# Optimization experiments

Hardware: AMD Instinct MI355X
Metric: run time of the kernel (lower is better)

Reference implementation:

```python
import jax, jax.numpy as jnp
from jax import lax
import numpy as np

B = 8192
NUM_CTX = 300; NUM_STN = 300; NUM_GPE = 20; NUM_GPI = 2; NUM_OUT = 20
FF_DIM = 20; FF_STEPS = 20; STN_ITERS = 50
ETA_GPE = 1.0; ETA_STN = 1.0 / 3.0; ETA_GPI = 0.1
A1 = 1.0; A2 = 1.0; THETAD1 = 0.0; THETAD2 = 0.0
UNITS = (64, 128, 64)

_SPECS = [("vf0", UNITS[0], NUM_CTX), ("vf1", UNITS[1], UNITS[0]), ("vf2", UNITS[2], UNITS[1]), ("vf3", 1, UNITS[2]),
          ("jd1", FF_DIM, NUM_CTX), ("jd2", FF_DIM, NUM_CTX), ("kd1", FF_DIM, NUM_CTX), ("kd2", FF_DIM, NUM_CTX),
          ("sg", NUM_GPE, NUM_STN), ("gs", NUM_STN, NUM_GPE), ("glat", NUM_GPE, NUM_GPE), ("slat", NUM_STN, NUM_STN),
          ("d1gpi", NUM_GPI, FF_DIM), ("stngpi", NUM_GPI, NUM_STN),
          ("ih", 4 * NUM_OUT, NUM_GPI), ("hh", 4 * NUM_OUT, NUM_OUT)]


def _lin_init(k, out_d, in_d):
    kw, kb = jax.random.split(k)
    bound = 1.0 / np.sqrt(in_d)
    w = jax.random.uniform(kw, (out_d, in_d), minval=-bound, maxval=bound, dtype=jnp.float32)
    b = jax.random.uniform(kb, (out_d,), minval=-bound, maxval=bound, dtype=jnp.float32)
    return w, b


def setup_inputs() -> dict:
    key = jax.random.key(0)
    ks = iter(jax.random.split(key, 40))
    inp = {}
    inp["stimulus"] = jax.random.normal(next(ks), (B, NUM_CTX), dtype=jnp.float32)
    inp["deltavf"] = jax.random.normal(next(ks), (B, 1), dtype=jnp.float32)
    inp["hx0"] = jax.random.uniform(next(ks), (B, NUM_OUT), dtype=jnp.float32)
    inp["cx0"] = jax.random.uniform(next(ks), (B, NUM_OUT), dtype=jnp.float32)
    for name, o, i in _SPECS:
        w, b = _lin_init(next(ks), o, i)
        inp["w_" + name] = w
        inp["b_" + name] = b
    return inp


def _lin(x, w, b):
    return x @ w.T + b


def _lstm_cell(x, h, c, w_ih, b_ih, w_hh, b_hh):
    gates = _lin(x, w_ih, b_ih) + _lin(h, w_hh, b_hh)
    i, f, g, o = jnp.split(gates, 4, axis=-1)  # torch LSTMCell gate order
    c_new = jax.nn.sigmoid(f) * c + jax.nn.sigmoid(i) * jnp.tanh(g)
    h_new = jax.nn.sigmoid(o) * jnp.tanh(c_new)
    return h_new, c_new


def reference(stimulus, deltavf, hx0, cx0,
              w_vf0, b_vf0, w_vf1, b_vf1, w_vf2, b_vf2, w_vf3, b_vf3,
              w_jd1, b_jd1, w_jd2, b_jd2, w_kd1, b_kd1, w_kd2, b_kd2,
              w_sg, b_sg, w_gs, b_gs, w_glat, b_glat, w_slat, b_slat,
              w_d1gpi, b_d1gpi, w_stngpi, b_stngpi,
              w_ih, b_ih, w_hh, b_hh):
    bsz = stimulus.shape[0]
    # value function head
    h = jax.nn.relu(_lin(stimulus, w_vf0, b_vf0))
    h = jax.nn.relu(_lin(h, w_vf1, b_vf1))
    h = jax.nn.relu(_lin(h, w_vf2, b_vf2))
    vt = jnp.tanh(_lin(h, w_vf3, b_vf3))  # [B, 1]

    lamd1 = jax.nn.sigmoid(A1 * (deltavf - THETAD1))  # [B, 1]
    lamd2 = jax.nn.sigmoid(A2 * (deltavf - THETAD2))  # [B, 1]

    # loop-invariant striatal drives (computed every iter in torch, same value)
    J_D1 = _lin(stimulus, w_jd1, b_jd1)
    J_D2 = _lin(stimulus, w_jd2, b_jd2)
    K_D1 = _lin(stimulus, w_kd1, b_kd1)
    K_D2 = _lin(stimulus, w_kd2, b_kd2)

    def ff_step(carry, _):
        v1, v2 = carry
        v1 = jax.nn.sigmoid(lamd1 * (J_D1 * (1.0 - v1) + (1.0 - K_D1) * v1))
        v2 = jax.nn.sigmoid(lamd2 * (J_D2 * (1.0 - v2) + (1.0 - K_D2) * v2))
        return (v1, v2), None

    z_ff = jnp.zeros((bsz, FF_DIM), dtype=stimulus.dtype)
    (V_D1, V_D2), _ = lax.scan(ff_step, (z_ff, z_ff), None, length=FF_STEPS)

    V_GPi_DP = _lin(V_D1, w_d1gpi, b_d1gpi)  # [B, num_gpi]

    def stn_step(carry, _):
        xgpe, xstn, vstn, vgpi, hx, cx = carry
        xgpe = xgpe + ETA_GPE * (-xgpe + _lin(vstn, w_sg, b_sg) + _lin(xgpe, w_glat, b_glat) - V_D2)
        xstn = xstn + ETA_STN * (-xstn + _lin(xgpe, w_gs, b_gs) + _lin(vstn, w_slat, b_slat))
        vstn = jnp.tanh(lamd2 * xstn)
        V_GPi_IP = lamd2 * _lin(vstn, w_stngpi, b_stngpi)
        vgpi = vgpi + ETA_GPI * (-vgpi - V_GPi_DP + 2.0 * V_GPi_IP)
        hx, cx = _lstm_cell(-vgpi, hx, cx, w_ih, b_ih, w_hh, b_hh)
        return (xgpe, xstn, vstn, vgpi, hx, cx), None

    carry0 = (jnp.zeros((bsz, NUM_GPE), dtype=stimulus.dtype),
              jnp.zeros((bsz, NUM_STN), dtype=stimulus.dtype),
              jnp.zeros((bsz, NUM_STN), dtype=stimulus.dtype),  # tanh(lamd2*0) = 0
              jnp.zeros((bsz, NUM_GPI), dtype=stimulus.dtype),
              hx0, cx0)
    carry, _ = lax.scan(stn_step, carry0, None, length=STN_ITERS)
    hx = carry[4]
    return hx, vt
```

## Files before the change

kernel.cpp:

```cpp
#include <hip/hip_runtime.h>


typedef _Float16 f16_t;
typedef _Float16 f16x8 __attribute__((ext_vector_type(8)));
typedef _Float16 f16x4 __attribute__((ext_vector_type(4)));
typedef float floatx4 __attribute__((ext_vector_type(4)));

#define BTOT 8192
#define BM   32
#define NTHR 512
#define NBLK 256
#define VSTR 328
#define XST  32

struct Params {
  const float *stimulus, *deltavf, *hx0, *cx0;
  const float *w_vf0, *b_vf0, *w_vf1, *b_vf1, *w_vf2, *b_vf2, *w_vf3, *b_vf3;
  const float *w_jd1, *b_jd1, *w_jd2, *b_jd2, *w_kd1, *b_kd1, *w_kd2, *b_kd2;
  const float *w_sg, *b_sg, *w_gs, *b_gs, *w_glat, *b_glat, *w_slat, *b_slat;
  const float *w_d1gpi, *b_d1gpi, *w_stngpi, *b_stngpi;
  const float *w_ih, *b_ih, *w_hh, *b_hh;
  float* out;
};

struct __align__(16) Smem {
  f16_t vstn[BM * VSTR];
  f16_t xgpe[2][BM * XST];
  f16_t hxf[BM * XST];
  f16_t wB2[21 * 512];
  union {
    f16_t h1f[BM * 128];
    float scr[2560];
    float gates[BM * 80];
  } u;
  float h0f[BM * 64];
  float V_D2f[BM * 20];
  float cxL[BM * 20], hxL[BM * 20];
  float bsumS[304];
  float bsg[20];
  float bihh[80], wih0[80], wih1[80];
  float DPs[BM * 2], vgpis[BM * 2], lamS[BM];
};

__device__ __forceinline__ float rcp_f(float x) { return __builtin_amdgcn_rcpf(x); }
__device__ __forceinline__ float sigm_fast(float x) { return rcp_f(1.f + __expf(-x)); }
__device__ __forceinline__ float tanh_fast(float x) { return 1.f - 2.f * rcp_f(1.f + __expf(2.f * x)); }

__device__ __forceinline__ f16x8 ldfrag(const float* row, int k0, int kmax, bool valid) {
  float4 z = make_float4(0.f, 0.f, 0.f, 0.f);
  int nv = valid ? (kmax - k0) : 0;
  float4 f0 = (nv >= 4) ? *(const float4*)(row + k0) : z;
  float4 f1 = (nv >= 8) ? *(const float4*)(row + k0 + 4) : z;
  f16x8 r;
  r[0] = (f16_t)f0.x; r[1] = (f16_t)f0.y; r[2] = (f16_t)f0.z; r[3] = (f16_t)f0.w;
  r[4] = (f16_t)f1.x; r[5] = (f16_t)f1.y; r[6] = (f16_t)f1.z; r[7] = (f16_t)f1.w;
  return r;
}

__global__ __launch_bounds__(NTHR, 2) void bg_main(Params P) {
  __shared__ Smem S;
  const int tid  = threadIdx.x;
  const int lane = tid & 63;
  const int wv   = tid >> 6;
  const int q    = lane >> 4;
  const int cl   = lane & 15;
  const int row0 = blockIdx.x * BM;
  const floatx4 zf = {0.f, 0.f, 0.f, 0.f};

  if (tid < BM) S.lamS[tid] = sigm_fast(P.deltavf[row0 + tid]);
  for (int i = tid; i < BM * 2; i += NTHR) S.vgpis[i] = 0.f;
  for (int i = tid; i < BM * VSTR; i += NTHR) S.vstn[i] = (f16_t)0.f;
  for (int i = tid; i < 2 * BM * XST; i += NTHR) ((f16_t*)S.xgpe)[i] = (f16_t)0.f;
  for (int i = tid; i < BM * XST; i += NTHR) {
    int m = i >> 5, j = i & 31;
    S.hxf[i] = (j < 20) ? (f16_t)P.hx0[row0 * 20 + m * 20 + j] : (f16_t)0.f;
  }
  for (int i = tid; i < BM * 20; i += NTHR) {
    S.cxL[i] = P.cx0[row0 * 20 + i];
    S.hxL[i] = P.hx0[row0 * 20 + i];
  }
  for (int i = tid; i < 21 * 512; i += NTHR) {
    int t = i >> 9, l = (i >> 3) & 63, jj = i & 7;
    int c2 = l & 15, k = ((l >> 4) << 3) + jj;
    float v = 0.f;
    if (t < 19) { int n = t * 16 + c2; if (n < 300 && k < 20) v = P.w_gs[n * 20 + k]; }
    else        { int g = (t - 19) * 16 + c2; if (g < 20 && k < 20) v = P.w_glat[g * 20 + k]; }
    S.wB2[i] = (f16_t)v;
  }
  for (int i = tid; i < 304; i += NTHR) S.bsumS[i] = (i < 300) ? (P.b_slat[i] + P.b_gs[i]) : 0.f;
  for (int i = tid; i < 20; i += NTHR)  S.bsg[i] = P.b_sg[i] + P.b_glat[i];
  for (int i = tid; i < 80; i += NTHR) {
    S.bihh[i] = P.b_ih[i] + P.b_hh[i];
    S.wih0[i] = P.w_ih[i * 2 + 0];
    S.wih1[i] = P.w_ih[i * 2 + 1];
  }

  {
    int o = tid & 63, mb = (tid >> 6) * 4;
    const float4* wr = (const float4*)(P.w_vf0 + o * 300);
    float bias = P.b_vf0[o], a[4];
#pragma unroll
    for (int u2 = 0; u2 < 4; ++u2) a[u2] = bias;
    for (int kq = 0; kq < 75; ++kq) {
      float4 w = wr[kq];
#pragma unroll
      for (int u2 = 0; u2 < 4; ++u2) {
        float4 v = *(const float4*)(P.stimulus + (size_t)(row0 + mb + u2) * 300 + kq * 4);
        a[u2] = fmaf(v.x, w.x, a[u2]); a[u2] = fmaf(v.y, w.y, a[u2]);
        a[u2] = fmaf(v.z, w.z, a[u2]); a[u2] = fmaf(v.w, w.w, a[u2]);
      }
    }
#pragma unroll
    for (int u2 = 0; u2 < 4; ++u2) S.h0f[(mb + u2) * 64 + o] = fmaxf(a[u2], 0.f);
  }
  __syncthreads();
  {
    int o = tid & 127, mb = (tid >> 7) * 8;
    const float* wr = P.w_vf1 + o * 64;
    float bias = P.b_vf1[o], a[8];
#pragma unroll
    for (int u2 = 0; u2 < 8; ++u2) a[u2] = bias;
    for (int k = 0; k < 64; ++k) {
      float w = wr[k];
#pragma unroll
      for (int u2 = 0; u2 < 8; ++u2) a[u2] = fmaf(S.h0f[(mb + u2) * 64 + k], w, a[u2]);
    }
#pragma unroll
    for (int u2 = 0; u2 < 8; ++u2) S.u.h1f[(mb + u2) * 128 + o] = (f16_t)fmaxf(a[u2], 0.f);
  }
  __syncthreads();
  {
    int o = tid & 63, mb = (tid >> 6) * 4;
    const float* wr = P.w_vf2 + o * 128;
    float bias = P.b_vf2[o], a[4];
#pragma unroll
    for (int u2 = 0; u2 < 4; ++u2) a[u2] = bias;
    for (int k = 0; k < 128; ++k) {
      float w = wr[k];
#pragma unroll
      for (int u2 = 0; u2 < 4; ++u2) a[u2] = fmaf((float)S.u.h1f[(mb + u2) * 128 + k], w, a[u2]);
    }
#pragma unroll
    for (int u2 = 0; u2 < 4; ++u2) S.h0f[(mb + u2) * 64 + o] = fmaxf(a[u2], 0.f);
  }
  __syncthreads();
  {
    int oid = tid & 127, mb = (tid >> 7) * 8;
    if (oid < 80) {
      int which = oid / 20, o = oid - which * 20;
      const float *wp, *bp;
      if (which == 0)      { wp = P.w_jd1; bp = P.b_jd1; }
      else if (which == 1) { wp = P.w_jd2; bp = P.b_jd2; }
      else if (which == 2) { wp = P.w_kd1; bp = P.b_kd1; }
      else                 { wp = P.w_kd2; bp = P.b_kd2; }
      float bias = bp[o], a[8];
#pragma unroll
      for (int u2 = 0; u2 < 8; ++u2) a[u2] = bias;
      for (int kq = 0; kq < 75; ++kq) {
        float4 w = *(const float4*)(wp + o * 300 + kq * 4);
#pragma unroll
        for (int u2 = 0; u2 < 8; ++u2) {
          float4 v = *(const float4*)(P.stimulus + (size_t)(row0 + mb + u2) * 300 + kq * 4);
          a[u2] = fmaf(v.x, w.x, a[u2]); a[u2] = fmaf(v.y, w.y, a[u2]);
          a[u2] = fmaf(v.z, w.z, a[u2]); a[u2] = fmaf(v.w, w.w, a[u2]);
        }
      }
#pragma unroll
      for (int u2 = 0; u2 < 8; ++u2) S.u.scr[which * 640 + (mb + u2) * 20 + o] = a[u2];
    }
    if (tid < BM) {
      float a = P.b_vf3[0];
      for (int k = 0; k < 64; ++k) a = fmaf(S.h0f[tid * 64 + k], P.w_vf3[k], a);
      P.out[(size_t)BTOT * 20 + row0 + tid] = tanh_fast(a);
    }
  }
  __syncthreads();
  for (int i = tid; i < BM * 20; i += NTHR) {
    int m = i / 20;
    float j1 = S.u.scr[i],        j2 = S.u.scr[640 + i];
    float k1 = S.u.scr[1280 + i], k2 = S.u.scr[1920 + i];
    float L = S.lamS[m], v1 = 0.f, v2 = 0.f;
    for (int s = 0; s < 20; ++s) {
      v1 = sigm_fast(L * (j1 * (1.f - v1) + (1.f - k1) * v1));
      v2 = sigm_fast(L * (j2 * (1.f - v2) + (1.f - k2) * v2));
    }
    S.V_D2f[i] = v2;
    S.h0f[i] = v1;
  }
  __syncthreads();
  if (tid < BM * 2) {
    int m = tid >> 1, p2 = tid & 1;
    float a = P.b_d1gpi[p2];
    for (int o = 0; o < 20; ++o) a = fmaf(S.h0f[m * 20 + o], P.w_d1gpi[p2 * 20 + o], a);
    S.DPs[tid] = a;
  }
  __syncthreads();

  f16x8 Wfr[30];
  if (wv < 7) {
#pragma unroll
    for (int j = 0; j < 3; ++j) {
      int t = wv + 7 * j;
      if (t < 19) {
        int n = t * 16 + cl;
#pragma unroll
        for (int c = 0; c < 10; ++c)
          Wfr[j * 10 + c] = ldfrag(P.w_slat + (size_t)(n < 300 ? n : 0) * 300, c * 32 + q * 8, 300, n < 300);
      } else {
        int g = (t - 19) * 16 + cl;
#pragma unroll
        for (int c = 0; c < 10; ++c)
          Wfr[j * 10 + c] = ldfrag(P.w_sg + (size_t)(g < 20 ? g : 0) * 300, c * 32 + q * 8, 300, g < 20);
      }
    }
  } else {
#pragma unroll
    for (int c = 0; c < 10; ++c)
      Wfr[c] = ldfrag(P.w_stngpi + (size_t)(cl < 2 ? cl : 0) * 300, c * 32 + q * 8, 300, cl < 2);
#pragma unroll
    for (int gt = 0; gt < 5; ++gt)
      Wfr[10 + gt] = ldfrag(P.w_hh + (size_t)(gt * 16 + cl) * 20, q * 8, 20, true);
    f16x8 z;
#pragma unroll
    for (int e = 0; e < 8; ++e) z[e] = (f16_t)0.f;
#pragma unroll
    for (int c = 15; c < 30; ++c) Wfr[c] = z;
  }
  const float bstn0 = P.b_stngpi[0], bstn1 = P.b_stngpi[1];

  float xs[3][2][4];
#pragma unroll
  for (int j = 0; j < 3; ++j)
#pragma unroll
    for (int mf = 0; mf < 2; ++mf)
#pragma unroll
      for (int r = 0; r < 4; ++r) xs[j][mf][r] = 0.f;

  const int cm = lane >> 1, cj0 = (lane & 1) * 10;

  auto consume = [&]() {
    floatx4 ip0 = zf, ip1 = zf;
#pragma unroll
    for (int c = 0; c < 10; ++c) {
      f16x8 b0 = *(const f16x8*)&S.vstn[cl * VSTR + c * 32 + q * 8];
      f16x8 b1 = *(const f16x8*)&S.vstn[(16 + cl) * VSTR + c * 32 + q * 8];
      ip0 = __builtin_amdgcn_mfma_f32_16x16x32_f16(Wfr[c], b0, ip0, 0, 0, 0);
      ip1 = __builtin_amdgcn_mfma_f32_16x16x32_f16(Wfr[c], b1, ip1, 0, 0, 0);
    }
    if (q == 0) {
#pragma unroll
      for (int mf = 0; mf < 2; ++mf) {
        int batch = cl + 16 * mf;
        float lm = S.lamS[batch];
#pragma unroll
        for (int p = 0; p < 2; ++p) {
          float raw = (mf ? ip1[p] : ip0[p]) + (p ? bstn1 : bstn0);
          int idx = batch * 2 + p;
          float v = S.vgpis[idx];
          v = v + 0.1f * (-v - S.DPs[idx] + 2.f * (lm * raw));
          S.vgpis[idx] = v;
        }
      }
    }
    f16x8 h0 = *(const f16x8*)&S.hxf[cl * XST + q * 8];
    f16x8 h1 = *(const f16x8*)&S.hxf[(16 + cl) * XST + q * 8];
    float vA0 = S.vgpis[cl * 2], vA1 = S.vgpis[cl * 2 + 1];
    float vB0 = S.vgpis[(cl + 16) * 2], vB1 = S.vgpis[(cl + 16) * 2 + 1];
#pragma unroll
    for (int gt = 0; gt < 5; ++gt) {
      floatx4 gA = __builtin_amdgcn_mfma_f32_16x16x32_f16(Wfr[10 + gt], h0, zf, 0, 0, 0);
      floatx4 gB = __builtin_amdgcn_mfma_f32_16x16x32_f16(Wfr[10 + gt], h1, zf, 0, 0, 0);
      int gb = gt * 16 + q * 4;
      floatx4 bi = *(const floatx4*)&S.bihh[gb];
      floatx4 w0 = *(const floatx4*)&S.wih0[gb];
      floatx4 w1 = *(const floatx4*)&S.wih1[gb];
#pragma unroll
      for (int r = 0; r < 4; ++r) {
        gA[r] += bi[r] - w0[r] * vA0 - w1[r] * vA1;
        gB[r] += bi[r] - w0[r] * vB0 - w1[r] * vB1;
      }
      *(floatx4*)&S.u.gates[cl * 80 + gb] = gA;
      *(floatx4*)&S.u.gates[(cl + 16) * 80 + gb] = gB;
    }
#pragma unroll
    for (int u2 = 0; u2 < 10; ++u2) {
      int j = cj0 + u2;
      float gi = S.u.gates[cm * 80 + j];
      float gf = S.u.gates[cm * 80 + 20 + j];
      float gg = S.u.gates[cm * 80 + 40 + j];
      float go = S.u.gates[cm * 80 + 60 + j];
      float cx = S.cxL[cm * 20 + j];
      float cn = sigm_fast(gf) * cx + sigm_fast(gi) * tanh_fast(gg);
      S.cxL[cm * 20 + j] = cn;
      float hn = sigm_fast(go) * tanh_fast(cn);
      S.hxL[cm * 20 + j] = hn;
      S.hxf[cm * XST + j] = (f16_t)hn;
    }
  };

  for (int it = 0; it < 50; ++it) {
    const int po = it & 1, pn = po ^ 1;
    floatx4 acc[3][2];
#pragma unroll
    for (int j = 0; j < 3; ++j) { acc[j][0] = zf; acc[j][1] = zf; }

    if (wv < 7) {
#pragma unroll
      for (int c = 0; c < 10; ++c) {
        f16x8 b0 = *(const f16x8*)&S.vstn[cl * VSTR + c * 32 + q * 8];
        f16x8 b1 = *(const f16x8*)&S.vstn[(16 + cl) * VSTR + c * 32 + q * 8];
#pragma unroll
        for (int j = 0; j < 3; ++j) {
          acc[j][0] = __builtin_amdgcn_mfma_f32_16x16x32_f16(Wfr[j * 10 + c], b0, acc[j][0], 0, 0, 0);
          acc[j][1] = __builtin_amdgcn_mfma_f32_16x16x32_f16(Wfr[j * 10 + c], b1, acc[j][1], 0, 0, 0);
        }
      }
      if (wv >= 5) {
        f16x8 Wg = *(const f16x8*)&S.wB2[(wv + 14) * 512 + lane * 8];
        f16x8 g0 = *(const f16x8*)&S.xgpe[po][cl * XST + q * 8];
        f16x8 g1 = *(const f16x8*)&S.xgpe[po][(16 + cl) * XST + q * 8];
        acc[2][0] = __builtin_amdgcn_mfma_f32_16x16x32_f16(Wg, g0, acc[2][0], 0, 0, 0);
        acc[2][1] = __builtin_amdgcn_mfma_f32_16x16x32_f16(Wg, g1, acc[2][1], 0, 0, 0);
        int g0i = (wv - 5) * 16 + q * 4;
        if (g0i < 20) {
          floatx4 bg4 = *(const floatx4*)&S.bsg[g0i];
#pragma unroll
          for (int mf = 0; mf < 2; ++mf) {
            int batch = cl + 16 * mf;
            floatx4 vd4 = *(const floatx4*)&S.V_D2f[batch * 20 + g0i];
            f16x4 pk;
#pragma unroll
            for (int r = 0; r < 4; ++r) pk[r] = (f16_t)(acc[2][mf][r] + bg4[r] - vd4[r]);
            *(f16x4*)&S.xgpe[pn][batch * XST + g0i] = pk;
          }
        }
      }
    } else if (it > 0) {
      consume();
    }
    __syncthreads();

    if (wv < 7) {
      f16x8 x0 = *(const f16x8*)&S.xgpe[pn][cl * XST + q * 8];
      f16x8 x1 = *(const f16x8*)&S.xgpe[pn][(16 + cl) * XST + q * 8];
#pragma unroll
      for (int j = 0; j < 3; ++j) {
        int t = wv + 7 * j;
        if (t < 19) {
          f16x8 Wg = *(const f16x8*)&S.wB2[t * 512 + lane * 8];
          acc[j][0] = __builtin_amdgcn_mfma_f32_16x16x32_f16(Wg, x0, acc[j][0], 0, 0, 0);
          acc[j][1] = __builtin_amdgcn_mfma_f32_16x16x32_f16(Wg, x1, acc[j][1], 0, 0, 0);
          int n0 = t * 16 + q * 4;
          if (!(t == 18 && q == 3)) {
            floatx4 bs4 = *(const floatx4*)&S.bsumS[n0];
#pragma unroll
            for (int mf = 0; mf < 2; ++mf) {
              float lm = S.lamS[cl + 16 * mf];
              f16x4 pk;
#pragma unroll
              for (int r = 0; r < 4; ++r) {
                float xo = xs[j][mf][r];
                float xn = xo + (1.0f / 3.0f) * (acc[j][mf][r] + bs4[r] - xo);
                xs[j][mf][r] = xn;
                pk[r] = (f16_t)tanh_fast(lm * xn);
              }
              *(f16x4*)&S.vstn[(cl + 16 * mf) * VSTR + n0] = pk;
            }
          }
        }
      }
    }
    __syncthreads();
  }

  if (wv == 7) {
    consume();
#pragma unroll
    for (int u2 = 0; u2 < 10; ++u2)
      P.out[(size_t)row0 * 20 + cm * 20 + cj0 + u2] = S.hxL[cm * 20 + cj0 + u2];
  }
}

extern "C" void kernel_launch(void* const* d_in, const int* in_sizes, int n_in,
                              void* d_out, int out_size, void* d_ws, size_t ws_size,
                              hipStream_t stream) {
  (void)in_sizes; (void)n_in; (void)out_size; (void)d_ws; (void)ws_size;
  Params P;
  P.stimulus = (const float*)d_in[0];
  P.deltavf  = (const float*)d_in[1];
  P.hx0 = (const float*)d_in[2];
  P.cx0 = (const float*)d_in[3];
  P.w_vf0 = (const float*)d_in[4];  P.b_vf0 = (const float*)d_in[5];
  P.w_vf1 = (const float*)d_in[6];  P.b_vf1 = (const float*)d_in[7];
  P.w_vf2 = (const float*)d_in[8];  P.b_vf2 = (const float*)d_in[9];
  P.w_vf3 = (const float*)d_in[10]; P.b_vf3 = (const float*)d_in[11];
  P.w_jd1 = (const float*)d_in[12]; P.b_jd1 = (const float*)d_in[13];
  P.w_jd2 = (const float*)d_in[14]; P.b_jd2 = (const float*)d_in[15];
  P.w_kd1 = (const float*)d_in[16]; P.b_kd1 = (const float*)d_in[17];
  P.w_kd2 = (const float*)d_in[18]; P.b_kd2 = (const float*)d_in[19];
  P.w_sg  = (const float*)d_in[20]; P.b_sg  = (const float*)d_in[21];
  P.w_gs  = (const float*)d_in[22]; P.b_gs  = (const float*)d_in[23];
  P.w_glat= (const float*)d_in[24]; P.b_glat= (const float*)d_in[25];
  P.w_slat= (const float*)d_in[26]; P.b_slat= (const float*)d_in[27];
  P.w_d1gpi  = (const float*)d_in[28]; P.b_d1gpi  = (const float*)d_in[29];
  P.w_stngpi = (const float*)d_in[30]; P.b_stngpi = (const float*)d_in[31];
  P.w_ih = (const float*)d_in[32]; P.b_ih = (const float*)d_in[33];
  P.w_hh = (const float*)d_in[34]; P.b_hh = (const float*)d_in[35];
  P.out  = (float*)d_out;
  bg_main<<<NBLK, NTHR, 0, stream>>>(P);
}
```

Before: 446.8 us.

## Double block to 1024 threads and spread STN tiles over 15 waves

Raises the block size from 8 to 16 waves. The 19 STN tiles and 2 GPe tiles of each iteration are now spread over 15 compute waves, each handling at most two tiles instead of three, and wave 15 runs the LSTM consumer. Because each wave no longer holds its tiles' xstn state in registers, that state moves into a new LDS array. The prologue dense layers are re-split so each thread handles fewer batch rows. The intent is more MFMA parallelism per iteration, at the cost of extra LDS traffic and footprint, and a launch-bounds hint that may tighten the register budget and cause spills.

```diff
diff --git a/kernel.cpp b/kernel.cpp
--- a/kernel.cpp
+++ b/kernel.cpp
@@ -8,7 +8,7 @@
 
 #define BTOT 8192
 #define BM   32
-#define NTHR 512
+#define NTHR 1024
 #define NBLK 256
 #define VSTR 328
 #define XST  32
@@ -28,6 +28,7 @@
   f16_t xgpe[2][BM * XST];
   f16_t hxf[BM * XST];
   f16_t wB2[21 * 512];
+  float xsL[21 * 512];
   union {
     f16_t h1f[BM * 128];
     float scr[2560];
@@ -57,7 +58,7 @@
   return r;
 }
 
-__global__ __launch_bounds__(NTHR, 2) void bg_main(Params P) {
+__global__ __launch_bounds__(NTHR, 4) void bg_main(Params P) {
   __shared__ Smem S;
   const int tid  = threadIdx.x;
   const int lane = tid & 63;
@@ -71,6 +72,7 @@
   for (int i = tid; i < BM * 2; i += NTHR) S.vgpis[i] = 0.f;
   for (int i = tid; i < BM * VSTR; i += NTHR) S.vstn[i] = (f16_t)0.f;
   for (int i = tid; i < 2 * BM * XST; i += NTHR) ((f16_t*)S.xgpe)[i] = (f16_t)0.f;
+  for (int i = tid; i < 21 * 512; i += NTHR) S.xsL[i] = 0.f;
   for (int i = tid; i < BM * XST; i += NTHR) {
     int m = i >> 5, j = i & 31;
     S.hxf[i] = (j < 20) ? (f16_t)P.hx0[row0 * 20 + m * 20 + j] : (f16_t)0.f;
@@ -96,56 +98,50 @@
   }
 
   {
-    int o = tid & 63, mb = (tid >> 6) * 4;
+    int o = tid & 63, mb = (tid >> 6) * 2;
     const float4* wr = (const float4*)(P.w_vf0 + o * 300);
-    float bias = P.b_vf0[o], a[4];
-#pragma unroll
-    for (int u2 = 0; u2 < 4; ++u2) a[u2] = bias;
+    float bias = P.b_vf0[o], a0 = bias, a1 = bias;
     for (int kq = 0; kq < 75; ++kq) {
       float4 w = wr[kq];
-#pragma unroll
-      for (int u2 = 0; u2 < 4; ++u2) {
-        float4 v = *(const float4*)(P.stimulus + (size_t)(row0 + mb + u2) * 300 + kq * 4);
-        a[u2] = fmaf(v.x, w.x, a[u2]); a[u2] = fmaf(v.y, w.y, a[u2]);
-        a[u2] = fmaf(v.z, w.z, a[u2]); a[u2] = fmaf(v.w, w.w, a[u2]);
-      }
-    }
-#pragma unroll
-    for (int u2 = 0; u2 < 4; ++u2) S.h0f[(mb + u2) * 64 + o] = fmaxf(a[u2], 0.f);
+      float4 v0 = *(const float4*)(P.stimulus + (size_t)(row0 + mb) * 300 + kq * 4);
+      float4 v1 = *(const float4*)(P.stimulus + (size_t)(row0 + mb + 1) * 300 + kq * 4);
+      a0 = fmaf(v0.x, w.x, a0); a0 = fmaf(v0.y, w.y, a0); a0 = fmaf(v0.z, w.z, a0); a0 = fmaf(v0.w, w.w, a0);
+      a1 = fmaf(v1.x, w.x, a1); a1 = fmaf(v1.y, w.y, a1); a1 = fmaf(v1.z, w.z, a1); a1 = fmaf(v1.w, w.w, a1);
+    }
+    S.h0f[(mb + 0) * 64 + o] = fmaxf(a0, 0.f);
+    S.h0f[(mb + 1) * 64 + o] = fmaxf(a1, 0.f);
   }
   __syncthreads();
   {
-    int o = tid & 127, mb = (tid >> 7) * 8;
+    int o = tid & 127, mb = (tid >> 7) * 4;
     const float* wr = P.w_vf1 + o * 64;
-    float bias = P.b_vf1[o], a[8];
-#pragma unroll
-    for (int u2 = 0; u2 < 8; ++u2) a[u2] = bias;
+    float bias = P.b_vf1[o], a[4];
+#pragma unroll
+    for (int u2 = 0; u2 < 4; ++u2) a[u2] = bias;
     for (int k = 0; k < 64; ++k) {
       float w = wr[k];
 #pragma unroll
-      for (int u2 = 0; u2 < 8; ++u2) a[u2] = fmaf(S.h0f[(mb + u2) * 64 + k], w, a[u2]);
-    }
-#pragma unroll
-    for (int u2 = 0; u2 < 8; ++u2) S.u.h1f[(mb + u2) * 128 + o] = (f16_t)fmaxf(a[u2], 0.f);
+      for (int u2 = 0; u2 < 4; ++u2) a[u2] = fmaf(S.h0f[(mb + u2) * 64 + k], w, a[u2]);
+    }
+#pragma unroll
+    for (int u2 = 0; u2 < 4; ++u2) S.u.h1f[(mb + u2) * 128 + o] = (f16_t)fmaxf(a[u2], 0.f);
   }
   __syncthreads();
   {
-    int o = tid & 63, mb = (tid >> 6) * 4;
+    int o = tid & 63, mb = (tid >> 6) * 2;
     const float* wr = P.w_vf2 + o * 128;
-    float bias = P.b_vf2[o], a[4];
-#pragma unroll
-    for (int u2 = 0; u2 < 4; ++u2) a[u2] = bias;
+    float bias = P.b_vf2[o], a0 = bias, a1 = bias;
     for (int k = 0; k < 128; ++k) {
       float w = wr[k];
-#pragma unroll
-      for (int u2 = 0; u2 < 4; ++u2) a[u2] = fmaf((float)S.u.h1f[(mb + u2) * 128 + k], w, a[u2]);
-    }
-#pragma unroll
-    for (int u2 = 0; u2 < 4; ++u2) S.h0f[(mb + u2) * 64 + o] = fmaxf(a[u2], 0.f);
+      a0 = fmaf((float)S.u.h1f[(mb + 0) * 128 + k], w, a0);
+      a1 = fmaf((float)S.u.h1f[(mb + 1) * 128 + k], w, a1);
+    }
+    S.h0f[(mb + 0) * 64 + o] = fmaxf(a0, 0.f);
+    S.h0f[(mb + 1) * 64 + o] = fmaxf(a1, 0.f);
   }
   __syncthreads();
   {
-    int oid = tid & 127, mb = (tid >> 7) * 8;
+    int oid = tid & 127, mb = (tid >> 7) * 4;
     if (oid < 80) {
       int which = oid / 20, o = oid - which * 20;
       const float *wp, *bp;
@@ -153,20 +149,20 @@
       else if (which == 1) { wp = P.w_jd2; bp = P.b_jd2; }
       else if (which == 2) { wp = P.w_kd1; bp = P.b_kd1; }
       else                 { wp = P.w_kd2; bp = P.b_kd2; }
-      float bias = bp[o], a[8];
-#pragma unroll
-      for (int u2 = 0; u2 < 8; ++u2) a[u2] = bias;
+      float bias = bp[o], a[4];
+#pragma unroll
+      for (int u2 = 0; u2 < 4; ++u2) a[u2] = bias;
       for (int kq = 0; kq < 75; ++kq) {
         float4 w = *(const float4*)(wp + o * 300 + kq * 4);
 #pragma unroll
-        for (int u2 = 0; u2 < 8; ++u2) {
+        for (int u2 = 0; u2 < 4; ++u2) {
           float4 v = *(const float4*)(P.stimulus + (size_t)(row0 + mb + u2) * 300 + kq * 4);
           a[u2] = fmaf(v.x, w.x, a[u2]); a[u2] = fmaf(v.y, w.y, a[u2]);
           a[u2] = fmaf(v.z, w.z, a[u2]); a[u2] = fmaf(v.w, w.w, a[u2]);
         }
       }
 #pragma unroll
-      for (int u2 = 0; u2 < 8; ++u2) S.u.scr[which * 640 + (mb + u2) * 20 + o] = a[u2];
+      for (int u2 = 0; u2 < 4; ++u2) S.u.scr[which * 640 + (mb + u2) * 20 + o] = a[u2];
     }
     if (tid < BM) {
       float a = P.b_vf3[0];
@@ -196,22 +192,23 @@
   }
   __syncthreads();
 
-  f16x8 Wfr[30];
-  if (wv < 7) {
-#pragma unroll
-    for (int j = 0; j < 3; ++j) {
-      int t = wv + 7 * j;
-      if (t < 19) {
-        int n = t * 16 + cl;
-#pragma unroll
-        for (int c = 0; c < 10; ++c)
-          Wfr[j * 10 + c] = ldfrag(P.w_slat + (size_t)(n < 300 ? n : 0) * 300, c * 32 + q * 8, 300, n < 300);
-      } else {
-        int g = (t - 19) * 16 + cl;
-#pragma unroll
-        for (int c = 0; c < 10; ++c)
-          Wfr[j * 10 + c] = ldfrag(P.w_sg + (size_t)(g < 20 ? g : 0) * 300, c * 32 + q * 8, 300, g < 20);
-      }
+  f16x8 Wfr[20];
+  const int t0 = wv, t1 = 15 + wv;
+  if (wv < 15) {
+    int n = t0 * 16 + cl;
+#pragma unroll
+    for (int c = 0; c < 10; ++c)
+      Wfr[c] = ldfrag(P.w_slat + (size_t)n * 300, c * 32 + q * 8, 300, true);
+    if (wv < 4) {
+      int n1 = t1 * 16 + cl;
+#pragma unroll
+      for (int c = 0; c < 10; ++c)
+        Wfr[10 + c] = ldfrag(P.w_slat + (size_t)(n1 < 300 ? n1 : 0) * 300, c * 32 + q * 8, 300, n1 < 300);
+    } else if (wv < 6) {
+      int g = (t1 - 19) * 16 + cl;
+#pragma unroll
+      for (int c = 0; c < 10; ++c)
+        Wfr[10 + c] = ldfrag(P.w_sg + (size_t)(g < 20 ? g : 0) * 300, c * 32 + q * 8, 300, g < 20);
     }
   } else {
 #pragma unroll
@@ -220,22 +217,8 @@
 #pragma unroll
     for (int gt = 0; gt < 5; ++gt)
       Wfr[10 + gt] = ldfrag(P.w_hh + (size_t)(gt * 16 + cl) * 20, q * 8, 20, true);
-    f16x8 z;
-#pragma unroll
-    for (int e = 0; e < 8; ++e) z[e] = (f16_t)0.f;
-#pragma unroll
-    for (int c = 15; c < 30; ++c) Wfr[c] = z;
   }
   const float bstn0 = P.b_stngpi[0], bstn1 = P.b_stngpi[1];
-
-  float xs[3][2][4];
-#pragma unroll
-  for (int j = 0; j < 3; ++j)
-#pragma unroll
-    for (int mf = 0; mf < 2; ++mf)
-#pragma unroll
-      for (int r = 0; r < 4; ++r) xs[j][mf][r] = 0.f;
-
   const int cm = lane >> 1, cj0 = (lane & 1) * 10;
 
   auto consume = [&]() {
@@ -298,30 +281,56 @@
     }
   };
 
+  auto phaseB_tile = [&](int t, floatx4* ac, const f16x8& x0, const f16x8& x1) {
+    f16x8 Wg = *(const f16x8*)&S.wB2[t * 512 + lane * 8];
+    ac[0] = __builtin_amdgcn_mfma_f32_16x16x32_f16(Wg, x0, ac[0], 0, 0, 0);
+    ac[1] = __builtin_amdgcn_mfma_f32_16x16x32_f16(Wg, x1, ac[1], 0, 0, 0);
+    int n0 = t * 16 + q * 4;
+    if (t == 18 && q == 3) return;
+    floatx4 bs4 = *(const floatx4*)&S.bsumS[n0];
+#pragma unroll
+    for (int mf = 0; mf < 2; ++mf) {
+      int batch = cl + 16 * mf;
+      float lm = S.lamS[batch];
+      float* xp = &S.xsL[t * 512 + batch * 16 + q * 4];
+      floatx4 xo4 = *(const floatx4*)xp;
+      f16x4 pk;
+      floatx4 xn4;
+#pragma unroll
+      for (int r = 0; r < 4; ++r) {
+        float xn = xo4[r] + (1.0f / 3.0f) * (ac[mf][r] + bs4[r] - xo4[r]);
+        xn4[r] = xn;
+        pk[r] = (f16_t)tanh_fast(lm * xn);
+      }
+      *(floatx4*)xp = xn4;
+      *(f16x4*)&S.vstn[batch * VSTR + n0] = pk;
+    }
+  };
+
   for (int it = 0; it < 50; ++it) {
     const int po = it & 1, pn = po ^ 1;
-    floatx4 acc[3][2];
-#pragma unroll
-    for (int j = 0; j < 3; ++j) { acc[j][0] = zf; acc[j][1] = zf; }
-
-    if (wv < 7) {
+    floatx4 a0[2], a1[2];
+    a0[0] = zf; a0[1] = zf; a1[0] = zf; a1[1] = zf;
+
+    if (wv < 15) {
 #pragma unroll
       for (int c = 0; c < 10; ++c) {
         f16x8 b0 = *(const f16x8*)&S.vstn[cl * VSTR + c * 32 + q * 8];
         f16x8 b1 = *(const f16x8*)&S.vstn[(16 + cl) * VSTR + c * 32 + q * 8];
-#pragma unroll
-        for (int j = 0; j < 3; ++j) {
-          acc[j][0] = __builtin_amdgcn_mfma_f32_16x16x32_f16(Wfr[j * 10 + c], b0, acc[j][0], 0, 0, 0);
-          acc[j][1] = __builtin_amdgcn_mfma_f32_16x16x32_f16(Wfr[j * 10 + c], b1, acc[j][1], 0, 0, 0);
+        a0[0] = __builtin_amdgcn_mfma_f32_16x16x32_f16(Wfr[c], b0, a0[0], 0, 0, 0);
+        a0[1] = __builtin_amdgcn_mfma_f32_16x16x32_f16(Wfr[c], b1, a0[1], 0, 0, 0);
+        if (wv < 6) {
+          a1[0] = __builtin_amdgcn_mfma_f32_16x16x32_f16(Wfr[10 + c], b0, a1[0], 0, 0, 0);
+          a1[1] = __builtin_amdgcn_mfma_f32_16x16x32_f16(Wfr[10 + c], b1, a1[1], 0, 0, 0);
         }
       }
-      if (wv >= 5) {
-        f16x8 Wg = *(const f16x8*)&S.wB2[(wv + 14) * 512 + lane * 8];
+      if (wv == 4 || wv == 5) {
+        f16x8 Wg = *(const f16x8*)&S.wB2[t1 * 512 + lane * 8];
         f16x8 g0 = *(const f16x8*)&S.xgpe[po][cl * XST + q * 8];
         f16x8 g1 = *(const f16x8*)&S.xgpe[po][(16 + cl) * XST + q * 8];
-        acc[2][0] = __builtin_amdgcn_mfma_f32_16x16x32_f16(Wg, g0, acc[2][0], 0, 0, 0);
-        acc[2][1] = __builtin_amdgcn_mfma_f32_16x16x32_f16(Wg, g1, acc[2][1], 0, 0, 0);
-        int g0i = (wv - 5) * 16 + q * 4;
+        a1[0] = __builtin_amdgcn_mfma_f32_16x16x32_f16(Wg, g0, a1[0], 0, 0, 0);
+        a1[1] = __builtin_amdgcn_mfma_f32_16x16x32_f16(Wg, g1, a1[1], 0, 0, 0);
+        int g0i = (t1 - 19) * 16 + q * 4;
         if (g0i < 20) {
           floatx4 bg4 = *(const floatx4*)&S.bsg[g0i];
 #pragma unroll
@@ -330,7 +339,7 @@
             floatx4 vd4 = *(const floatx4*)&S.V_D2f[batch * 20 + g0i];
             f16x4 pk;
 #pragma unroll
-            for (int r = 0; r < 4; ++r) pk[r] = (f16_t)(acc[2][mf][r] + bg4[r] - vd4[r]);
+            for (int r = 0; r < 4; ++r) pk[r] = (f16_t)(a1[mf][r] + bg4[r] - vd4[r]);
             *(f16x4*)&S.xgpe[pn][batch * XST + g0i] = pk;
           }
         }
@@ -340,40 +349,16 @@
     }
     __syncthreads();
 
-    if (wv < 7) {
+    if (wv < 15) {
       f16x8 x0 = *(const f16x8*)&S.xgpe[pn][cl * XST + q * 8];
       f16x8 x1 = *(const f16x8*)&S.xgpe[pn][(16 + cl) * XST + q * 8];
-#pragma unroll
-      for (int j = 0; j < 3; ++j) {
-        int t = wv + 7 * j;
-        if (t < 19) {
-          f16x8 Wg = *(const f16x8*)&S.wB2[t * 512 + lane * 8];
-          acc[j][0] = __builtin_amdgcn_mfma_f32_16x16x32_f16(Wg, x0, acc[j][0], 0, 0, 0);
-          acc[j][1] = __builtin_amdgcn_mfma_f32_16x16x32_f16(Wg, x1, acc[j][1], 0, 0, 0);
-          int n0 = t * 16 + q * 4;
-          if (!(t == 18 && q == 3)) {
-            floatx4 bs4 = *(const floatx4*)&S.bsumS[n0];
-#pragma unroll
-            for (int mf = 0; mf < 2; ++mf) {
-              float lm = S.lamS[cl + 16 * mf];
-              f16x4 pk;
-#pragma unroll
-              for (int r = 0; r < 4; ++r) {
-                float xo = xs[j][mf][r];
-                float xn = xo + (1.0f / 3.0f) * (acc[j][mf][r] + bs4[r] - xo);
-                xs[j][mf][r] = xn;
-                pk[r] = (f16_t)tanh_fast(lm * xn);
-              }
-              *(f16x4*)&S.vstn[(cl + 16 * mf) * VSTR + n0] = pk;
-            }
-          }
-        }
-      }
+      phaseB_tile(t0, a0, x0, x1);
+      if (wv < 4) phaseB_tile(t1, a1, x0, x1);
     }
     __syncthreads();
   }
 
-  if (wv == 7) {
+  if (wv == 15) {
     consume();
 #pragma unroll
     for (int u2 = 0; u2 < 10; ++u2)
```

After: 575.4 us. 1.29x slower.
